# Kernel optimization log

Hardware: AMD Instinct MI355X
Metric: run time of the kernel (lower is better)

## Reference

```python
import jax, jax.numpy as jnp
import numpy as np

N, F_IN, H, C, E, G, OUT = 50000, 128, 4, 64, 800000, 128, 8

def _glorot(key, shape):
    lim = float(np.sqrt(6.0 / (shape[0] + shape[-1] if len(shape) == 2 else shape[-1] + 1)))
    return jax.random.uniform(key, shape, jnp.float32, -lim, lim)

def setup_inputs() -> dict:
    key = jax.random.key(0)
    ks = jax.random.split(key, 12)
    x = jax.random.normal(ks[0], (N, F_IN), jnp.float32)
    edge_index = jax.random.randint(ks[1], (2, E), 0, N, jnp.int64)
    batch = jnp.sort(jax.random.randint(ks[2], (N,), 0, G, jnp.int64))
    return {
        "x": x, "edge_index": edge_index, "batch": batch,
        "W1": _glorot(ks[3], (F_IN, H * C)),
        "a1s": _glorot(ks[4], (H, C)), "a1d": _glorot(ks[5], (H, C)),
        "b1": jnp.zeros((H * C,), jnp.float32),
        "W2": _glorot(ks[6], (H * C, H * C)),
        "a2s": _glorot(ks[7], (H, C)), "a2d": _glorot(ks[8], (H, C)),
        "b2": jnp.zeros((C,), jnp.float32),
        "fc_w": _glorot(ks[9], (C, OUT)),
        "fc_b": jnp.zeros((OUT,), jnp.float32),
    }

def _gat_conv(x, src, dst, W, a_src, a_dst, bias, concat):
    # x: [N, in]; src/dst: [E'] (self-loops already appended, PyG default)
    n = x.shape[0]
    h = (x @ W).reshape(n, H, C)                       # [N, H, C]
    alpha_src = (h * a_src).sum(-1)                    # [N, H]
    alpha_dst = (h * a_dst).sum(-1)                    # [N, H]
    e = alpha_src[src] + alpha_dst[dst]                # [E', H]
    e = jax.nn.leaky_relu(e, 0.2)
    # neighbor softmax grouped by destination node
    m = jax.ops.segment_max(e, dst, num_segments=n)    # [N, H]
    ex = jnp.exp(e - m[dst])
    denom = jax.ops.segment_sum(ex, dst, num_segments=n)
    alpha = ex / (denom[dst] + 1e-16)                  # [E', H]
    msg = h[src] * alpha[:, :, None]                   # [E', H, C]
    out = jax.ops.segment_sum(msg, dst, num_segments=n)  # [N, H, C]
    out = out.reshape(n, H * C) if concat else out.mean(axis=1)
    return out + bias

def reference(x, edge_index, batch, W1, a1s, a1d, b1, W2, a2s, a2d, b2, fc_w, fc_b):
    n = x.shape[0]
    loop = jnp.arange(n, dtype=edge_index.dtype)
    src = jnp.concatenate([edge_index[0], loop])
    dst = jnp.concatenate([edge_index[1], loop])
    h = _gat_conv(x, src, dst, W1, a1s, a1d, b1, concat=True)
    h = jax.nn.elu(h)                                  # activation, dropout p=0
    h = _gat_conv(h, src, dst, W2, a2s, a2d, b2, concat=False)
    # global mean pool over graphs
    sums = jax.ops.segment_sum(h, batch, num_segments=G)
    cnts = jax.ops.segment_sum(jnp.ones((n,), h.dtype), batch, num_segments=G)
    pooled = sums / jnp.maximum(cnts, 1.0)[:, None]    # [G, C]
    return pooled @ fc_w + fc_b                        # [G, OUT]
```

## Files before the change

kernel.cpp:

```cpp
#include <hip/hip_runtime.h>
#include <hip/hip_bf16.h>
#include <cstddef>
#include <cstdint>

#define NN 50000
#define MPAD 50048
#define F_IN 128
#define NH 4
#define NC 64
#define NE 800000
#define NG 128
#define NOUT 8
#define HC 256
#define EP (NE + NN)

typedef unsigned short ushort_t;
typedef _Float16 f16;
typedef __attribute__((ext_vector_type(2))) _Float16 f16x2;
typedef __attribute__((ext_vector_type(8))) _Float16 f16x8;
typedef __attribute__((ext_vector_type(4))) float f32x4;

__device__ __forceinline__ float lrelu02(float x) { return x > 0.0f ? x : 0.2f * x; }
__device__ __forceinline__ float elu1(float x)    { return x > 0.0f ? x : expm1f(x); }

__device__ __forceinline__ ushort_t f2h_bits(float f) {
    f16 h = (f16)f;
    union { f16 h; ushort_t u; } cv; cv.h = h;
    return cv.u;
}
__device__ __forceinline__ uint32_t pack2h(float a, float b) {
    union { f16 h[2]; uint32_t u; } cv;
    cv.h[0] = (f16)a; cv.h[1] = (f16)b;
    return cv.u;
}
__device__ __forceinline__ f16x2 as_h2(uint32_t q) {
    union { uint32_t u; f16x2 h; } cv; cv.u = q;
    return cv.h;
}
__device__ __forceinline__ void h2_unpack(uint32_t q, float& lo, float& hi) {
    union { uint32_t u; f16 h[2]; } cv; cv.u = q;
    lo = (float)cv.h[0];
    hi = (float)cv.h[1];
}

__device__ __forceinline__ float fdot2f(f16x2 a, f16x2 b, float c) {
#if __has_builtin(__builtin_amdgcn_fdot2)
    return __builtin_amdgcn_fdot2(a, b, c, false);
#else
    float d;
    asm("v_dot2_f32_f16 %0, %1, %2, %3" : "=v"(d) : "v"(a), "v"(b), "v"(c));
    return d;
#endif
}
__device__ __forceinline__ uint32_t permb(uint32_t a, uint32_t b, uint32_t s) {
    return __builtin_amdgcn_perm(a, b, s);
}
#define SEL_E 0x01000504u
#define SEL_O 0x03020706u

__device__ __forceinline__ void gld16(const void* g, void* l) {
    __builtin_amdgcn_global_load_lds(
        (const __attribute__((address_space(1))) unsigned int*)g,
        (__attribute__((address_space(3))) unsigned int*)l, 16, 0, 0);
}

#define XN4 (NN * F_IN / 4)
#define NW (F_IN * HC + HC * HC)
__global__ void prep_kernel(const int* __restrict__ edst,
                            const float* __restrict__ x,
                            const float* __restrict__ W1,
                            const float* __restrict__ W2,
                            int* __restrict__ deg,
                            f16* __restrict__ xh,
                            f16* __restrict__ w1t, f16* __restrict__ w2t) {
    int idx = blockIdx.x * blockDim.x + threadIdx.x;
    if (idx < EP) {
        int d = (idx < NE) ? edst[idx] : (idx - NE);
        atomicAdd(&deg[d], 1);
        return;
    }
    idx -= EP;
    if (idx < XN4) {
        float4 v = ((const float4*)x)[idx];
        f16 o[4] = {(f16)v.x, (f16)v.y, (f16)v.z, (f16)v.w};
        *(uint2*)(xh + idx * 4) = *(const uint2*)o;
        return;
    }
    idx -= XN4;
    const int n1 = F_IN * HC;
    if (idx < n1) {
        int k = idx / HC, n = idx % HC;
        w1t[n * F_IN + k] = (f16)W1[idx];
    } else if (idx < NW) {
        int i2 = idx - n1;
        int k = i2 / HC, n = i2 % HC;
        w2t[n * HC + k] = (f16)W2[i2];
    }
}

__global__ __launch_bounds__(256) void scan_p1(const int* __restrict__ deg,
                                               int* __restrict__ partials) {
    __shared__ int lds[256];
    int b = blockIdx.x, t = threadIdx.x;
    int i0 = b * 1024 + t * 4;
    int s = 0;
#pragma unroll
    for (int j = 0; j < 4; j++) { int i = i0 + j; if (i < NN) s += deg[i]; }
    lds[t] = s;
    __syncthreads();
    for (int o = 128; o; o >>= 1) { if (t < o) lds[t] += lds[t + o]; __syncthreads(); }
    if (t == 0) partials[b] = lds[0];
}

__global__ __launch_bounds__(256) void scan_p3(const int* __restrict__ deg,
                                               const int* __restrict__ partials,
                                               int* __restrict__ offs) {
    __shared__ int lds[256];
    __shared__ int base_s;
    int b = blockIdx.x, t = threadIdx.x;
    if (t == 0) {
        int s = 0;
        for (int i = 0; i < b; i++) s += partials[i];
        base_s = s;
        if (b == 0) offs[0] = 0;
    }
    int i0 = b * 1024 + t * 4;
    int v[4]; int s = 0;
#pragma unroll
    for (int j = 0; j < 4; j++) { int i = i0 + j; v[j] = (i < NN) ? deg[i] : 0; s += v[j]; }
    lds[t] = s;
    __syncthreads();
    for (int o = 1; o < 256; o <<= 1) {
        int x = (t >= o) ? lds[t - o] : 0;
        __syncthreads();
        lds[t] += x;
        __syncthreads();
    }
    int run = base_s + (lds[t] - s);
#pragma unroll
    for (int j = 0; j < 4; j++) { run += v[j]; int i = i0 + j; if (i < NN) offs[i + 1] = run; }
}

__global__ void edge_fill(const int* __restrict__ esrc, const int* __restrict__ edst,
                          const int* __restrict__ offs, int* __restrict__ fill,
                          int* __restrict__ csr) {
    int e = blockIdx.x * blockDim.x + threadIdx.x;
    if (e >= EP) return;
    int s, d;
    if (e < NE) { s = esrc[e]; d = edst[e]; } else { s = d = e - NE; }
    int pos = offs[d] + atomicAdd(&fill[d], 1);
    csr[pos] = s;
}

__global__ __launch_bounds__(256, 3) void gemm_gat(
        const f16* __restrict__ A, const f16* __restrict__ BT,
        const float* __restrict__ a_s, const float* __restrict__ a_d,
        ushort_t* __restrict__ hf2, float* __restrict__ asrc,
        float* __restrict__ adst, int M, int K) {
    __shared__ alignas(16) char smem[33792];
    f16* lA = (f16*)smem;
    f16* lB = (f16*)smem + 4096;

    int t = threadIdx.x;
    int wave = t >> 6, lane = t & 63;
    int wm = wave >> 1, wn = wave & 1;
    int quad = lane >> 4, l15 = lane & 15;
    int tileM = blockIdx.x * 128;
    int by = blockIdx.y;

    f32x4 acc[4][4];
#pragma unroll
    for (int f = 0; f < 4; f++)
#pragma unroll
        for (int g = 0; g < 4; g++) acc[f][g] = (f32x4){0.f, 0.f, 0.f, 0.f};

    for (int k0 = 0; k0 < K; k0 += 32) {
        __syncthreads();
#pragma unroll
        for (int i = 0; i < 2; i++) {
            int c = wave * 2 + i;
            int row = c * 16 + (lane >> 2);
            int kk = k0 + (lane & 3) * 8;
            gld16(A + (size_t)(tileM + row) * K + kk, &lA[c * 512]);
            gld16(BT + (size_t)(by * 128 + row) * K + kk, &lB[c * 512]);
        }
        __syncthreads();

        f16x8 ah[4], bh[4];
#pragma unroll
        for (int f = 0; f < 4; f++)
            ah[f] = *(const f16x8*)&lA[(wm * 64 + f * 16 + l15) * 32 + quad * 8];
#pragma unroll
        for (int g = 0; g < 4; g++)
            bh[g] = *(const f16x8*)&lB[(wn * 64 + g * 16 + l15) * 32 + quad * 8];
#pragma unroll
        for (int f = 0; f < 4; f++)
#pragma unroll
            for (int g = 0; g < 4; g++)
                acc[f][g] = __builtin_amdgcn_mfma_f32_16x16x32_f16(ah[f], bh[g], acc[f][g], 0, 0, 0);
    }

    int head = (by << 1) | wn;
    float as_v[4], ad_v[4];
#pragma unroll
    for (int g = 0; g < 4; g++) {
        as_v[g] = a_s[head * 64 + g * 16 + l15];
        ad_v[g] = a_d[head * 64 + g * 16 + l15];
    }
#pragma unroll
    for (int f = 0; f < 4; f++) {
#pragma unroll
        for (int r = 0; r < 4; r++) {
            float ps = acc[f][0][r] * as_v[0] + acc[f][1][r] * as_v[1]
                     + acc[f][2][r] * as_v[2] + acc[f][3][r] * as_v[3];
            float pd = acc[f][0][r] * ad_v[0] + acc[f][1][r] * ad_v[1]
                     + acc[f][2][r] * ad_v[2] + acc[f][3][r] * ad_v[3];
#pragma unroll
            for (int o = 1; o < 16; o <<= 1) {
                ps += __shfl_xor(ps, o);
                pd += __shfl_xor(pd, o);
            }
            int row = tileM + wm * 64 + f * 16 + quad * 4 + r;
            if (l15 == 0 && row < M) {
                asrc[row * 4 + head] = ps;
                adst[row * 4 + head] = pd;
            }
        }
    }

    __syncthreads();
    ushort_t* lC2u = (ushort_t*)smem;
    const uint32_t* lC2d = (const uint32_t*)smem;
#pragma unroll
    for (int f = 0; f < 4; f++)
#pragma unroll
        for (int g = 0; g < 4; g++)
#pragma unroll
            for (int r = 0; r < 4; r++)
                lC2u[(wm * 64 + f * 16 + quad * 4 + r) * 132 + (g * 16 + l15) * 2 + wn] =
                    f2h_bits(acc[f][g][r]);
    __syncthreads();
    uint32_t* hb2 = (uint32_t*)hf2;
#pragma unroll
    for (int it = 0; it < 32; it++) {
        int row = wave * 32 + it;
        uint32_t v = lC2d[row * 66 + lane];
        hb2[(size_t)(tileM + row) * 128 + by * 64 + lane] = v;
    }
}

template <int CONCAT>
__device__ void gat_node_fullwave(const ushort_t* __restrict__ hf2,
                                  const float* __restrict__ asrc,
                                  const float* __restrict__ adst,
                                  const int* __restrict__ offs,
                                  const int* __restrict__ csr,
                                  const float* __restrict__ bias,
                                  f16* __restrict__ oh,
                                  float* __restrict__ of,
                                  int node, int lane, uint2* lwF) {
    int start = offs[node];
    int deg = offs[node + 1] - start;
    float4 ad = *(const float4*)(adst + node * 4);

    float w0, w1, w2, w3;
    float m0, m1, m2, m3, i0, i1, i2, i3;
    int msrc = 0;

    if (deg <= 64) {
        float t0 = -1e30f, t1 = -1e30f, t2 = -1e30f, t3 = -1e30f;
        if (lane < deg) {
            int sidx = csr[start + lane];
            float4 as = *(const float4*)(asrc + sidx * 4);
            t0 = lrelu02(as.x + ad.x);
            t1 = lrelu02(as.y + ad.y);
            t2 = lrelu02(as.z + ad.z);
            t3 = lrelu02(as.w + ad.w);
            msrc = sidx;
        }
        m0 = t0; m1 = t1; m2 = t2; m3 = t3;
#pragma unroll
        for (int o = 1; o < 64; o <<= 1) {
            m0 = fmaxf(m0, __shfl_xor(m0, o));
            m1 = fmaxf(m1, __shfl_xor(m1, o));
            m2 = fmaxf(m2, __shfl_xor(m2, o));
            m3 = fmaxf(m3, __shfl_xor(m3, o));
        }
        w0 = __expf(t0 - m0);
        w1 = __expf(t1 - m1);
        w2 = __expf(t2 - m2);
        w3 = __expf(t3 - m3);
        float s0 = w0, s1 = w1, s2 = w2, s3 = w3;
#pragma unroll
        for (int o = 1; o < 64; o <<= 1) {
            s0 += __shfl_xor(s0, o);
            s1 += __shfl_xor(s1, o);
            s2 += __shfl_xor(s2, o);
            s3 += __shfl_xor(s3, o);
        }
        i0 = 1.0f / (s0 + 1e-16f);
        i1 = 1.0f / (s1 + 1e-16f);
        i2 = 1.0f / (s2 + 1e-16f);
        i3 = 1.0f / (s3 + 1e-16f);
        w0 *= i0; w1 *= i1; w2 *= i2; w3 *= i3;
    } else {
        m0 = m1 = m2 = m3 = -1e30f;
        float s0 = 0.f, s1 = 0.f, s2 = 0.f, s3 = 0.f;
        float e0 = 0.f, e1 = 0.f, e2 = 0.f, e3 = 0.f;
        for (int j = lane; j < deg; j += 64) {
            int sidx = csr[start + j];
            float4 as = *(const float4*)(asrc + sidx * 4);
            float t0 = lrelu02(as.x + ad.x);
            float t1 = lrelu02(as.y + ad.y);
            float t2 = lrelu02(as.z + ad.z);
            float t3 = lrelu02(as.w + ad.w);
            if (j == lane) { e0 = t0; e1 = t1; e2 = t2; e3 = t3; msrc = sidx; }
            float nm;
            nm = fmaxf(m0, t0); s0 = s0 * __expf(m0 - nm) + __expf(t0 - nm); m0 = nm;
            nm = fmaxf(m1, t1); s1 = s1 * __expf(m1 - nm) + __expf(t1 - nm); m1 = nm;
            nm = fmaxf(m2, t2); s2 = s2 * __expf(m2 - nm) + __expf(t2 - nm); m2 = nm;
            nm = fmaxf(m3, t3); s3 = s3 * __expf(m3 - nm) + __expf(t3 - nm); m3 = nm;
        }
        for (int o = 32; o; o >>= 1) {
            float om, os, nm;
            om = __shfl_xor(m0, o); os = __shfl_xor(s0, o);
            nm = fmaxf(m0, om); s0 = s0 * __expf(m0 - nm) + os * __expf(om - nm); m0 = nm;
            om = __shfl_xor(m1, o); os = __shfl_xor(s1, o);
            nm = fmaxf(m1, om); s1 = s1 * __expf(m1 - nm) + os * __expf(om - nm); m1 = nm;
            om = __shfl_xor(m2, o); os = __shfl_xor(s2, o);
            nm = fmaxf(m2, om); s2 = s2 * __expf(m2 - nm) + os * __expf(om - nm); m2 = nm;
            om = __shfl_xor(m3, o); os = __shfl_xor(s3, o);
            nm = fmaxf(m3, om); s3 = s3 * __expf(m3 - nm) + os * __expf(om - nm); m3 = nm;
        }
        i0 = 1.0f / (s0 + 1e-16f);
        i1 = 1.0f / (s1 + 1e-16f);
        i2 = 1.0f / (s2 + 1e-16f);
        i3 = 1.0f / (s3 + 1e-16f);
        w0 = __expf(e0 - m0) * i0;
        w1 = __expf(e1 - m1) * i1;
        w2 = __expf(e2 - m2) * i2;
        w3 = __expf(e3 - m3) * i3;
    }

    lwF[lane] = (uint2){pack2h(w0, w1), pack2h(w2, w3)};

    int hp = lane >> 5;
    const uint32_t* lwu = (const uint32_t*)lwF;
    float aE0 = 0.f, aO0 = 0.f, aE1 = 0.f, aO1 = 0.f;
    float c0a = 0.f, c0b = 0.f, c1a = 0.f, c1b = 0.f;
    const uint32_t* hb = (const uint32_t*)hf2 + lane * 2;
    int jmax = deg < 64 ? deg : 64;

    int j = 0;
    if (CONCAT) {
        for (; j + 4 <= jmax; j += 4) {
            int s0 = __builtin_amdgcn_readlane(msrc, j);
            int s1 = __builtin_amdgcn_readlane(msrc, j + 1);
            int s2 = __builtin_amdgcn_readlane(msrc, j + 2);
            int s3 = __builtin_amdgcn_readlane(msrc, j + 3);
            uint2 q0 = *(const uint2*)(hb + (size_t)s0 * 128);
            uint2 q1 = *(const uint2*)(hb + (size_t)s1 * 128);
            uint2 q2 = *(const uint2*)(hb + (size_t)s2 * 128);
            uint2 q3 = *(const uint2*)(hb + (size_t)s3 * 128);
            uint32_t wA = lwu[(j + 0) * 2 + hp];
            uint32_t wB = lwu[(j + 1) * 2 + hp];
            uint32_t wC = lwu[(j + 2) * 2 + hp];
            uint32_t wD = lwu[(j + 3) * 2 + hp];
            uint32_t weAB = permb(wA, wB, SEL_E), woAB = permb(wA, wB, SEL_O);
            uint32_t weCD = permb(wC, wD, SEL_E), woCD = permb(wC, wD, SEL_O);
            uint32_t xeAB = permb(q0.x, q1.x, SEL_E), xoAB = permb(q0.x, q1.x, SEL_O);
            uint32_t yeAB = permb(q0.y, q1.y, SEL_E), yoAB = permb(q0.y, q1.y, SEL_O);
            uint32_t xeCD = permb(q2.x, q3.x, SEL_E), xoCD = permb(q2.x, q3.x, SEL_O);
            uint32_t yeCD = permb(q2.y, q3.y, SEL_E), yoCD = permb(q2.y, q3.y, SEL_O);
            aE0 = fdot2f(as_h2(xeAB), as_h2(weAB), aE0);
            aO0 = fdot2f(as_h2(xoAB), as_h2(woAB), aO0);
            aE1 = fdot2f(as_h2(yeAB), as_h2(weAB), aE1);
            aO1 = fdot2f(as_h2(yoAB), as_h2(woAB), aO1);
            aE0 = fdot2f(as_h2(xeCD), as_h2(weCD), aE0);
            aO0 = fdot2f(as_h2(xoCD), as_h2(woCD), aO0);
            aE1 = fdot2f(as_h2(yeCD), as_h2(weCD), aE1);
            aO1 = fdot2f(as_h2(yoCD), as_h2(woCD), aO1);
        }
        for (; j < jmax; j++) {
            int sidx = __builtin_amdgcn_readlane(msrc, j);
            f16x2 wh = as_h2(lwu[j * 2 + hp]);
            uint2 q = *(const uint2*)(hb + (size_t)sidx * 128);
            f16x2 qx = as_h2(q.x), qy = as_h2(q.y);
            aE0 += (float)qx[0] * (float)wh[0];
            aO0 += (float)qx[1] * (float)wh[1];
            aE1 += (float)qy[0] * (float)wh[0];
            aO1 += (float)qy[1] * (float)wh[1];
        }
    } else {
        for (; j + 4 <= jmax; j += 4) {
            int s0 = __builtin_amdgcn_readlane(msrc, j);
            int s1 = __builtin_amdgcn_readlane(msrc, j + 1);
            int s2 = __builtin_amdgcn_readlane(msrc, j + 2);
            int s3 = __builtin_amdgcn_readlane(msrc, j + 3);
            uint2 q0 = *(const uint2*)(hb + (size_t)s0 * 128);
            uint2 q1 = *(const uint2*)(hb + (size_t)s1 * 128);
            uint2 q2 = *(const uint2*)(hb + (size_t)s2 * 128);
            uint2 q3 = *(const uint2*)(hb + (size_t)s3 * 128);
            f16x2 w0v = as_h2(lwu[(j + 0) * 2 + hp]);
            f16x2 w1v = as_h2(lwu[(j + 1) * 2 + hp]);
            f16x2 w2v = as_h2(lwu[(j + 2) * 2 + hp]);
            f16x2 w3v = as_h2(lwu[(j + 3) * 2 + hp]);
            c0a = fdot2f(as_h2(q0.x), w0v, c0a);
            c1a = fdot2f(as_h2(q0.y), w0v, c1a);
            c0b = fdot2f(as_h2(q1.x), w1v, c0b);
            c1b = fdot2f(as_h2(q1.y), w1v, c1b);
            c0a = fdot2f(as_h2(q2.x), w2v, c0a);
            c1a = fdot2f(as_h2(q2.y), w2v, c1a);
            c0b = fdot2f(as_h2(q3.x), w3v, c0b);
            c1b = fdot2f(as_h2(q3.y), w3v, c1b);
        }
        for (; j < jmax; j++) {
            int sidx = __builtin_amdgcn_readlane(msrc, j);
            f16x2 wh = as_h2(lwu[j * 2 + hp]);
            uint2 q = *(const uint2*)(hb + (size_t)sidx * 128);
            c0a = fdot2f(as_h2(q.x), wh, c0a);
            c1a = fdot2f(as_h2(q.y), wh, c1a);
        }
    }
    for (int jj = 64; jj < deg; jj++) {
        int sidx = csr[start + jj];
        float4 as = *(const float4*)(asrc + sidx * 4);
        float u0 = __expf(lrelu02(as.x + ad.x) - m0) * i0;
        float u1 = __expf(lrelu02(as.y + ad.y) - m1) * i1;
        float u2 = __expf(lrelu02(as.z + ad.z) - m2) * i2;
        float u3 = __expf(lrelu02(as.w + ad.w) - m3) * i3;
        float ue = hp ? u2 : u0;
        float uo = hp ? u3 : u1;
        uint2 q = *(const uint2*)(hb + (size_t)sidx * 128);
        float xl, xh2, yl, yh;
        h2_unpack(q.x, xl, xh2);
        h2_unpack(q.y, yl, yh);
        if (CONCAT) {
            aE0 += ue * xl;
            aO0 += uo * xh2;
            aE1 += ue * yl;
            aO1 += uo * yh;
        } else {
            c0a += ue * xl + uo * xh2;
            c1a += ue * yl + uo * yh;
        }
    }

    int c0 = (lane & 31) * 2;
    int he = hp * 2, ho = hp * 2 + 1;
    if (CONCAT) {
        size_t base = (size_t)node * HC;
        float vE0 = elu1(aE0 + bias[he * 64 + c0]);
        float vE1 = elu1(aE1 + bias[he * 64 + c0 + 1]);
        float vO0 = elu1(aO0 + bias[ho * 64 + c0]);
        float vO1 = elu1(aO1 + bias[ho * 64 + c0 + 1]);
        f16 pe[2] = {(f16)vE0, (f16)vE1};
        f16 po[2] = {(f16)vO0, (f16)vO1};
        *(uint32_t*)(oh + base + he * 64 + c0) = *(const uint32_t*)pe;
        *(uint32_t*)(oh + base + ho * 64 + c0) = *(const uint32_t*)po;
    } else {
        float s0 = c0a + c0b;
        float s1 = c1a + c1b;
        s0 += __shfl_xor(s0, 32);
        s1 += __shfl_xor(s1, 32);
        if (hp == 0) {
            float2 v = {0.25f * s0 + bias[c0], 0.25f * s1 + bias[c0 + 1]};
            *(float2*)(of + (size_t)node * NC + c0) = v;
        }
    }
}

template <int CONCAT>
__global__ __launch_bounds__(256) void gat_agg(const ushort_t* __restrict__ hf2,
                                               const float* __restrict__ asrc,
                                               const float* __restrict__ adst,
                                               const int* __restrict__ offs,
                                               const int* __restrict__ csr,
                                               const float* __restrict__ bias,
                                               f16* __restrict__ oh,
                                               float* __restrict__ of) {
    __shared__ uint4 lw4[4][64];
    int wave = threadIdx.x >> 6, lane = threadIdx.x & 63;
    int grp = lane >> 5, l31 = lane & 31;
    int hp = (lane >> 4) & 1;
    int nbase = blockIdx.x * 8 + wave * 2;
    int node = nbase + grp;
    int start = offs[node];
    int deg = offs[node + 1] - start;

    if (!__all(deg <= 32)) {
        uint2* lwF = (uint2*)&lw4[wave][0];
        gat_node_fullwave<CONCAT>(hf2, asrc, adst, offs, csr, bias, oh, of,
                                  nbase, lane, lwF);
        gat_node_fullwave<CONCAT>(hf2, asrc, adst, offs, csr, bias, oh, of,
                                  nbase + 1, lane, lwF);
        return;
    }

    float4 ad = *(const float4*)(adst + (size_t)node * 4);
    float t0 = -1e30f, t1 = -1e30f, t2 = -1e30f, t3 = -1e30f;
    int msrc = 0;
    if (l31 < deg) {
        int sidx = csr[start + l31];
        float4 as = *(const float4*)(asrc + (size_t)sidx * 4);
        t0 = lrelu02(as.x + ad.x);
        t1 = lrelu02(as.y + ad.y);
        t2 = lrelu02(as.z + ad.z);
        t3 = lrelu02(as.w + ad.w);
        msrc = sidx;
    }
    float m0 = t0, m1 = t1, m2 = t2, m3 = t3;
#pragma unroll
    for (int o = 1; o < 32; o <<= 1) {
        m0 = fmaxf(m0, __shfl_xor(m0, o));
        m1 = fmaxf(m1, __shfl_xor(m1, o));
        m2 = fmaxf(m2, __shfl_xor(m2, o));
        m3 = fmaxf(m3, __shfl_xor(m3, o));
    }
    float w0 = __expf(t0 - m0);
    float w1 = __expf(t1 - m1);
    float w2 = __expf(t2 - m2);
    float w3 = __expf(t3 - m3);
    float s0 = w0, s1 = w1, s2 = w2, s3 = w3;
#pragma unroll
    for (int o = 1; o < 32; o <<= 1) {
        s0 += __shfl_xor(s0, o);
        s1 += __shfl_xor(s1, o);
        s2 += __shfl_xor(s2, o);
        s3 += __shfl_xor(s3, o);
    }
    w0 *= 1.0f / (s0 + 1e-16f);
    w1 *= 1.0f / (s1 + 1e-16f);
    w2 *= 1.0f / (s2 + 1e-16f);
    w3 *= 1.0f / (s3 + 1e-16f);

    lw4[wave][lane] = (uint4){(uint32_t)msrc, pack2h(w0, w1),
                              (uint32_t)msrc, pack2h(w2, w3)};

    const uint2* lwp = (const uint2*)&lw4[wave][grp * 32];
    const uint4* hq = (const uint4*)hf2;
    int c0 = (l31 & 15) * 4;

    if (CONCAT) {
        float aE0 = 0.f, aE1 = 0.f, aE2 = 0.f, aE3 = 0.f;
        float aO0 = 0.f, aO1 = 0.f, aO2 = 0.f, aO3 = 0.f;
        int j = 0;
        for (; j + 2 <= deg; j += 2) {
            uint2 e0 = lwp[(j + 0) * 2 + hp];
            uint2 e1 = lwp[(j + 1) * 2 + hp];
            uint4 q0 = hq[(size_t)e0.x * 32 + l31];
            uint4 q1 = hq[(size_t)e1.x * 32 + l31];
            uint32_t we = permb(e0.y, e1.y, SEL_E);
            uint32_t wo = permb(e0.y, e1.y, SEL_O);
            aE0 = fdot2f(as_h2(permb(q0.x, q1.x, SEL_E)), as_h2(we), aE0);
            aO0 = fdot2f(as_h2(permb(q0.x, q1.x, SEL_O)), as_h2(wo), aO0);
            aE1 = fdot2f(as_h2(permb(q0.y, q1.y, SEL_E)), as_h2(we), aE1);
            aO1 = fdot2f(as_h2(permb(q0.y, q1.y, SEL_O)), as_h2(wo), aO1);
            aE2 = fdot2f(as_h2(permb(q0.z, q1.z, SEL_E)), as_h2(we), aE2);
            aO2 = fdot2f(as_h2(permb(q0.z, q1.z, SEL_O)), as_h2(wo), aO2);
            aE3 = fdot2f(as_h2(permb(q0.w, q1.w, SEL_E)), as_h2(we), aE3);
            aO3 = fdot2f(as_h2(permb(q0.w, q1.w, SEL_O)), as_h2(wo), aO3);
        }
        if (j < deg) {
            uint2 e0 = lwp[j * 2 + hp];
            uint4 q0 = hq[(size_t)e0.x * 32 + l31];
            f16x2 wh = as_h2(e0.y);
            f16x2 v;
            v = as_h2(q0.x); aE0 += (float)v[0] * (float)wh[0]; aO0 += (float)v[1] * (float)wh[1];
            v = as_h2(q0.y); aE1 += (float)v[0] * (float)wh[0]; aO1 += (float)v[1] * (float)wh[1];
            v = as_h2(q0.z); aE2 += (float)v[0] * (float)wh[0]; aO2 += (float)v[1] * (float)wh[1];
            v = as_h2(q0.w); aE3 += (float)v[0] * (float)wh[0]; aO3 += (float)v[1] * (float)wh[1];
        }
        int he = hp * 2, ho = hp * 2 + 1;
        size_t base = (size_t)node * HC;
        float4 bE = *(const float4*)(bias + he * 64 + c0);
        float4 bO = *(const float4*)(bias + ho * 64 + c0);
        f16 pe[4] = {(f16)elu1(aE0 + bE.x), (f16)elu1(aE1 + bE.y),
                     (f16)elu1(aE2 + bE.z), (f16)elu1(aE3 + bE.w)};
        f16 po[4] = {(f16)elu1(aO0 + bO.x), (f16)elu1(aO1 + bO.y),
                     (f16)elu1(aO2 + bO.z), (f16)elu1(aO3 + bO.w)};
        *(uint2*)(oh + base + he * 64 + c0) = *(const uint2*)pe;
        *(uint2*)(oh + base + ho * 64 + c0) = *(const uint2*)po;
    } else {
        float a0 = 0.f, a1 = 0.f, a2 = 0.f, a3 = 0.f;
        float b0 = 0.f, b1 = 0.f, b2 = 0.f, b3 = 0.f;
        int j = 0;
        for (; j + 2 <= deg; j += 2) {
            uint2 e0 = lwp[(j + 0) * 2 + hp];
            uint2 e1 = lwp[(j + 1) * 2 + hp];
            uint4 q0 = hq[(size_t)e0.x * 32 + l31];
            uint4 q1 = hq[(size_t)e1.x * 32 + l31];
            f16x2 wv0 = as_h2(e0.y), wv1 = as_h2(e1.y);
            a0 = fdot2f(as_h2(q0.x), wv0, a0);
            a1 = fdot2f(as_h2(q0.y), wv0, a1);
            a2 = fdot2f(as_h2(q0.z), wv0, a2);
            a3 = fdot2f(as_h2(q0.w), wv0, a3);
            b0 = fdot2f(as_h2(q1.x), wv1, b0);
            b1 = fdot2f(as_h2(q1.y), wv1, b1);
            b2 = fdot2f(as_h2(q1.z), wv1, b2);
            b3 = fdot2f(as_h2(q1.w), wv1, b3);
        }
        if (j < deg) {
            uint2 e0 = lwp[j * 2 + hp];
            uint4 q0 = hq[(size_t)e0.x * 32 + l31];
            f16x2 wv0 = as_h2(e0.y);
            a0 = fdot2f(as_h2(q0.x), wv0, a0);
            a1 = fdot2f(as_h2(q0.y), wv0, a1);
            a2 = fdot2f(as_h2(q0.z), wv0, a2);
            a3 = fdot2f(as_h2(q0.w), wv0, a3);
        }
        float u0 = a0 + b0, u1 = a1 + b1, u2 = a2 + b2, u3 = a3 + b3;
        u0 += __shfl_xor(u0, 16);
        u1 += __shfl_xor(u1, 16);
        u2 += __shfl_xor(u2, 16);
        u3 += __shfl_xor(u3, 16);
        if (hp == 0) {
            float4 bv = *(const float4*)(bias + c0);
            float4 v = {0.25f * u0 + bv.x, 0.25f * u1 + bv.y,
                        0.25f * u2 + bv.z, 0.25f * u3 + bv.w};
            *(float4*)(of + (size_t)node * NC + c0) = v;
        }
    }
}

__global__ __launch_bounds__(256) void pool_kernel(const float* __restrict__ out2,
                                                   const int* __restrict__ batch,
                                                   float* __restrict__ pool,
                                                   float* __restrict__ cnt) {
    int gw = (blockIdx.x * blockDim.x + threadIdx.x) >> 6;
    int lane = threadIdx.x & 63;
    int start = gw * 16;
    if (start >= NN) return;
    int end = start + 16 < NN ? start + 16 : NN;
    int curg = batch[start];
    float acc = 0.f; int run = 0;
    for (int node = start; node < end; node++) {
        int g = batch[node];
        if (g != curg) {
            atomicAdd(&pool[curg * 64 + lane], acc);
            if (lane == 0) atomicAdd(&cnt[curg], (float)run);
            curg = g; acc = 0.f; run = 0;
        }
        acc += out2[(size_t)node * NC + lane];
        run++;
    }
    atomicAdd(&pool[curg * 64 + lane], acc);
    if (lane == 0) atomicAdd(&cnt[curg], (float)run);
}

__global__ void fc_kernel(const float* __restrict__ pool, const float* __restrict__ cnt,
                          const float* __restrict__ fc_w, const float* __restrict__ fc_b,
                          float* __restrict__ out) {
    int idx = blockIdx.x * blockDim.x + threadIdx.x;
    if (idx >= NG * NOUT) return;
    int g = idx >> 3, o = idx & 7;
    float inv = 1.0f / fmaxf(cnt[g], 1.0f);
    float s = 0.f;
#pragma unroll
    for (int c = 0; c < 64; c++) s += pool[g * 64 + c] * fc_w[c * 8 + o];
    out[idx] = s * inv + fc_b[o];
}

extern "C" void kernel_launch(void* const* d_in, const int* in_sizes, int n_in,
                              void* d_out, int out_size, void* d_ws, size_t ws_size,
                              hipStream_t stream) {
    const float* x    = (const float*)d_in[0];
    const int*   ei   = (const int*)d_in[1];
    const int*   batch= (const int*)d_in[2];
    const float* W1   = (const float*)d_in[3];
    const float* a1s  = (const float*)d_in[4];
    const float* a1d  = (const float*)d_in[5];
    const float* b1   = (const float*)d_in[6];
    const float* W2   = (const float*)d_in[7];
    const float* a2s  = (const float*)d_in[8];
    const float* a2d  = (const float*)d_in[9];
    const float* b2   = (const float*)d_in[10];
    const float* fc_w = (const float*)d_in[11];
    const float* fc_b = (const float*)d_in[12];
    float* out = (float*)d_out;

    char* p = (char*)d_ws;
    auto alloc = [&](size_t bytes) -> char* {
        char* r = p; p += (bytes + 255) & ~(size_t)255; return r;
    };
    int*   deg     = (int*)alloc((size_t)NN * 4);
    int*   fill    = (int*)alloc((size_t)NN * 4);
    float* pool    = (float*)alloc((size_t)NG * 64 * 4);
    float* cnt     = (float*)alloc((size_t)NG * 4);
    size_t zero_bytes = (size_t)(p - (char*)d_ws);
    int*   offs    = (int*)alloc((size_t)(NN + 1) * 4);
    int*   partials= (int*)alloc(64 * 4);
    int*   csr     = (int*)alloc((size_t)EP * 4);
    float* asrc    = (float*)alloc((size_t)NN * 4 * 4);
    float* adst    = (float*)alloc((size_t)NN * 4 * 4);
    ushort_t* hf2  = (ushort_t*)alloc((size_t)MPAD * HC * 2);
    f16*   xh      = (f16*)alloc((size_t)MPAD * F_IN * 2);
    f16*   act     = (f16*)alloc((size_t)MPAD * HC * 2);
    f16*   w1t     = (f16*)alloc((size_t)HC * F_IN * 2);
    f16*   w2t     = (f16*)alloc((size_t)HC * HC * 2);
    float* out2    = (float*)xh;

    hipMemsetAsync(d_ws, 0, zero_bytes, stream);

    int prep_n = EP + XN4 + NW;
    prep_kernel<<<(prep_n + 255) / 256, 256, 0, stream>>>(
        ei + NE, x, W1, W2, deg, xh, w1t, w2t);
    scan_p1<<<49, 256, 0, stream>>>(deg, partials);
    scan_p3<<<49, 256, 0, stream>>>(deg, partials, offs);
    edge_fill<<<(EP + 255) / 256, 256, 0, stream>>>(ei, ei + NE, offs, fill, csr);

    dim3 gg((NN + 127) / 128, HC / 128);
    int nb8 = (NN + 7) / 8;

    gemm_gat<<<gg, 256, 0, stream>>>(xh, w1t, a1s, a1d, hf2, asrc, adst, NN, F_IN);
    gat_agg<1><<<nb8, 256, 0, stream>>>(hf2, asrc, adst, offs, csr, b1, act, nullptr);
    gemm_gat<<<gg, 256, 0, stream>>>(act, w2t, a2s, a2d, hf2, asrc, adst, NN, HC);
    gat_agg<0><<<nb8, 256, 0, stream>>>(hf2, asrc, adst, offs, csr, b2, nullptr, out2);
    pool_kernel<<<((NN + 15) / 16 + 3) / 4, 256, 0, stream>>>(out2, batch, pool, cnt);
    fc_kernel<<<(NG * NOUT + 255) / 256, 256, 0, stream>>>(pool, cnt, fc_w, fc_b, out);
}
```

Before: 370.6 us.

## Software-pipeline neighbor feature gathers in GAT aggregation with early prefetch

The first four neighbor feature rows are now gathered straight after the CSR index load, before the attention softmax runs, so their latency overlaps the softmax math. The aggregation loop is rewritten as a 4-deep pipeline that issues the next pair of gathers between FMA blocks. Padding slots get zero weight and index 0 so no tail loop is needed, at the cost of wasted loads on padded slots. An occupancy hint (launch_bounds 256,8) caps register use, which may cause spills given the extra live registers.

```diff
diff --git a/kernel.cpp b/kernel.cpp
--- a/kernel.cpp
+++ b/kernel.cpp
@@ -471,14 +471,14 @@
 }
 
 template <int CONCAT>
-__global__ __launch_bounds__(256) void gat_agg(const ushort_t* __restrict__ hf2,
-                                               const float* __restrict__ asrc,
-                                               const float* __restrict__ adst,
-                                               const int* __restrict__ offs,
-                                               const int* __restrict__ csr,
-                                               const float* __restrict__ bias,
-                                               f16* __restrict__ oh,
-                                               float* __restrict__ of) {
+__global__ __launch_bounds__(256, 8) void gat_agg(const ushort_t* __restrict__ hf2,
+                                                  const float* __restrict__ asrc,
+                                                  const float* __restrict__ adst,
+                                                  const int* __restrict__ offs,
+                                                  const int* __restrict__ csr,
+                                                  const float* __restrict__ bias,
+                                                  f16* __restrict__ oh,
+                                                  float* __restrict__ of) {
     __shared__ uint4 lw4[4][64];
     int wave = threadIdx.x >> 6, lane = threadIdx.x & 63;
     int grp = lane >> 5, l31 = lane & 31;
@@ -497,17 +497,29 @@
         return;
     }
 
+    const uint4* hq = (const uint4*)hf2;
+    int msrc = 0;
+    bool act = l31 < deg;
+    if (act) msrc = csr[start + l31];
+
+    int b0 = grp * 32;
+    int i0 = __shfl(msrc, b0 + 0);
+    int i1 = __shfl(msrc, b0 + 1);
+    int i2 = __shfl(msrc, b0 + 2);
+    int i3 = __shfl(msrc, b0 + 3);
+    uint4 q0 = hq[(uint32_t)i0 * 32u + l31];
+    uint4 q1 = hq[(uint32_t)i1 * 32u + l31];
+    uint4 q2 = hq[(uint32_t)i2 * 32u + l31];
+    uint4 q3 = hq[(uint32_t)i3 * 32u + l31];
+
     float4 ad = *(const float4*)(adst + (size_t)node * 4);
     float t0 = -1e30f, t1 = -1e30f, t2 = -1e30f, t3 = -1e30f;
-    int msrc = 0;
-    if (l31 < deg) {
-        int sidx = csr[start + l31];
-        float4 as = *(const float4*)(asrc + (size_t)sidx * 4);
+    if (act) {
+        float4 as = *(const float4*)(asrc + (size_t)msrc * 4);
         t0 = lrelu02(as.x + ad.x);
         t1 = lrelu02(as.y + ad.y);
         t2 = lrelu02(as.z + ad.z);
         t3 = lrelu02(as.w + ad.w);
-        msrc = sidx;
     }
     float m0 = t0, m1 = t1, m2 = t2, m3 = t3;
 #pragma unroll
@@ -538,38 +550,61 @@
                               (uint32_t)msrc, pack2h(w2, w3)};
 
     const uint2* lwp = (const uint2*)&lw4[wave][grp * 32];
-    const uint4* hq = (const uint4*)hf2;
     int c0 = (l31 & 15) * 4;
+    int deg4 = (deg + 3) & ~3;
+
+    uint32_t wy0 = lwp[0 * 2 + hp].y;
+    uint32_t wy1 = lwp[1 * 2 + hp].y;
+    uint32_t wy2 = lwp[2 * 2 + hp].y;
+    uint32_t wy3 = lwp[3 * 2 + hp].y;
 
     if (CONCAT) {
         float aE0 = 0.f, aE1 = 0.f, aE2 = 0.f, aE3 = 0.f;
         float aO0 = 0.f, aO1 = 0.f, aO2 = 0.f, aO3 = 0.f;
         int j = 0;
-        for (; j + 2 <= deg; j += 2) {
-            uint2 e0 = lwp[(j + 0) * 2 + hp];
-            uint2 e1 = lwp[(j + 1) * 2 + hp];
-            uint4 q0 = hq[(size_t)e0.x * 32 + l31];
-            uint4 q1 = hq[(size_t)e1.x * 32 + l31];
-            uint32_t we = permb(e0.y, e1.y, SEL_E);
-            uint32_t wo = permb(e0.y, e1.y, SEL_O);
-            aE0 = fdot2f(as_h2(permb(q0.x, q1.x, SEL_E)), as_h2(we), aE0);
-            aO0 = fdot2f(as_h2(permb(q0.x, q1.x, SEL_O)), as_h2(wo), aO0);
-            aE1 = fdot2f(as_h2(permb(q0.y, q1.y, SEL_E)), as_h2(we), aE1);
-            aO1 = fdot2f(as_h2(permb(q0.y, q1.y, SEL_O)), as_h2(wo), aO1);
-            aE2 = fdot2f(as_h2(permb(q0.z, q1.z, SEL_E)), as_h2(we), aE2);
-            aO2 = fdot2f(as_h2(permb(q0.z, q1.z, SEL_O)), as_h2(wo), aO2);
-            aE3 = fdot2f(as_h2(permb(q0.w, q1.w, SEL_E)), as_h2(we), aE3);
-            aO3 = fdot2f(as_h2(permb(q0.w, q1.w, SEL_O)), as_h2(wo), aO3);
-        }
-        if (j < deg) {
-            uint2 e0 = lwp[j * 2 + hp];
-            uint4 q0 = hq[(size_t)e0.x * 32 + l31];
-            f16x2 wh = as_h2(e0.y);
-            f16x2 v;
-            v = as_h2(q0.x); aE0 += (float)v[0] * (float)wh[0]; aO0 += (float)v[1] * (float)wh[1];
-            v = as_h2(q0.y); aE1 += (float)v[0] * (float)wh[0]; aO1 += (float)v[1] * (float)wh[1];
-            v = as_h2(q0.z); aE2 += (float)v[0] * (float)wh[0]; aO2 += (float)v[1] * (float)wh[1];
-            v = as_h2(q0.w); aE3 += (float)v[0] * (float)wh[0]; aO3 += (float)v[1] * (float)wh[1];
+        for (;;) {
+            int jn = j + 4;
+            bool more = jn < deg4;
+            {
+                uint32_t we = permb(wy0, wy1, SEL_E);
+                uint32_t wo = permb(wy0, wy1, SEL_O);
+                aE0 = fdot2f(as_h2(permb(q0.x, q1.x, SEL_E)), as_h2(we), aE0);
+                aO0 = fdot2f(as_h2(permb(q0.x, q1.x, SEL_O)), as_h2(wo), aO0);
+                aE1 = fdot2f(as_h2(permb(q0.y, q1.y, SEL_E)), as_h2(we), aE1);
+                aO1 = fdot2f(as_h2(permb(q0.y, q1.y, SEL_O)), as_h2(wo), aO1);
+                aE2 = fdot2f(as_h2(permb(q0.z, q1.z, SEL_E)), as_h2(we), aE2);
+                aO2 = fdot2f(as_h2(permb(q0.z, q1.z, SEL_O)), as_h2(wo), aO2);
+                aE3 = fdot2f(as_h2(permb(q0.w, q1.w, SEL_E)), as_h2(we), aE3);
+                aO3 = fdot2f(as_h2(permb(q0.w, q1.w, SEL_O)), as_h2(wo), aO3);
+            }
+            if (more) {
+                uint2 n0 = lwp[(jn + 0) * 2 + hp];
+                uint2 n1 = lwp[(jn + 1) * 2 + hp];
+                wy0 = n0.y; wy1 = n1.y;
+                q0 = hq[n0.x * 32u + l31];
+                q1 = hq[n1.x * 32u + l31];
+            }
+            {
+                uint32_t we = permb(wy2, wy3, SEL_E);
+                uint32_t wo = permb(wy2, wy3, SEL_O);
+                aE0 = fdot2f(as_h2(permb(q2.x, q3.x, SEL_E)), as_h2(we), aE0);
+                aO0 = fdot2f(as_h2(permb(q2.x, q3.x, SEL_O)), as_h2(wo), aO0);
+                aE1 = fdot2f(as_h2(permb(q2.y, q3.y, SEL_E)), as_h2(we), aE1);
+                aO1 = fdot2f(as_h2(permb(q2.y, q3.y, SEL_O)), as_h2(wo), aO1);
+                aE2 = fdot2f(as_h2(permb(q2.z, q3.z, SEL_E)), as_h2(we), aE2);
+                aO2 = fdot2f(as_h2(permb(q2.z, q3.z, SEL_O)), as_h2(wo), aO2);
+                aE3 = fdot2f(as_h2(permb(q2.w, q3.w, SEL_E)), as_h2(we), aE3);
+                aO3 = fdot2f(as_h2(permb(q2.w, q3.w, SEL_O)), as_h2(wo), aO3);
+            }
+            if (more) {
+                uint2 n2 = lwp[(jn + 2) * 2 + hp];
+                uint2 n3 = lwp[(jn + 3) * 2 + hp];
+                wy2 = n2.y; wy3 = n3.y;
+                q2 = hq[n2.x * 32u + l31];
+                q3 = hq[n3.x * 32u + l31];
+            }
+            if (!more) break;
+            j = jn;
         }
         int he = hp * 2, ho = hp * 2 + 1;
         size_t base = (size_t)node * HC;
@@ -583,33 +618,51 @@
         *(uint2*)(oh + base + ho * 64 + c0) = *(const uint2*)po;
     } else {
         float a0 = 0.f, a1 = 0.f, a2 = 0.f, a3 = 0.f;
-        float b0 = 0.f, b1 = 0.f, b2 = 0.f, b3 = 0.f;
+        float b0f = 0.f, b1f = 0.f, b2f = 0.f, b3f = 0.f;
         int j = 0;
-        for (; j + 2 <= deg; j += 2) {
-            uint2 e0 = lwp[(j + 0) * 2 + hp];
-            uint2 e1 = lwp[(j + 1) * 2 + hp];
-            uint4 q0 = hq[(size_t)e0.x * 32 + l31];
-            uint4 q1 = hq[(size_t)e1.x * 32 + l31];
-            f16x2 wv0 = as_h2(e0.y), wv1 = as_h2(e1.y);
-            a0 = fdot2f(as_h2(q0.x), wv0, a0);
-            a1 = fdot2f(as_h2(q0.y), wv0, a1);
-            a2 = fdot2f(as_h2(q0.z), wv0, a2);
-            a3 = fdot2f(as_h2(q0.w), wv0, a3);
-            b0 = fdot2f(as_h2(q1.x), wv1, b0);
-            b1 = fdot2f(as_h2(q1.y), wv1, b1);
-            b2 = fdot2f(as_h2(q1.z), wv1, b2);
-            b3 = fdot2f(as_h2(q1.w), wv1, b3);
-        }
-        if (j < deg) {
-            uint2 e0 = lwp[j * 2 + hp];
-            uint4 q0 = hq[(size_t)e0.x * 32 + l31];
-            f16x2 wv0 = as_h2(e0.y);
-            a0 = fdot2f(as_h2(q0.x), wv0, a0);
-            a1 = fdot2f(as_h2(q0.y), wv0, a1);
-            a2 = fdot2f(as_h2(q0.z), wv0, a2);
-            a3 = fdot2f(as_h2(q0.w), wv0, a3);
-        }
-        float u0 = a0 + b0, u1 = a1 + b1, u2 = a2 + b2, u3 = a3 + b3;
+        for (;;) {
+            int jn = j + 4;
+            bool more = jn < deg4;
+            {
+                f16x2 wvA = as_h2(wy0), wvB = as_h2(wy1);
+                a0 = fdot2f(as_h2(q0.x), wvA, a0);
+                a1 = fdot2f(as_h2(q0.y), wvA, a1);
+                a2 = fdot2f(as_h2(q0.z), wvA, a2);
+                a3 = fdot2f(as_h2(q0.w), wvA, a3);
+                b0f = fdot2f(as_h2(q1.x), wvB, b0f);
+                b1f = fdot2f(as_h2(q1.y), wvB, b1f);
+                b2f = fdot2f(as_h2(q1.z), wvB, b2f);
+                b3f = fdot2f(as_h2(q1.w), wvB, b3f);
+            }
+            if (more) {
+                uint2 n0 = lwp[(jn + 0) * 2 + hp];
+                uint2 n1 = lwp[(jn + 1) * 2 + hp];
+                wy0 = n0.y; wy1 = n1.y;
+                q0 = hq[n0.x * 32u + l31];
+                q1 = hq[n1.x * 32u + l31];
+            }
+            {
+                f16x2 wvC = as_h2(wy2), wvD = as_h2(wy3);
+                a0 = fdot2f(as_h2(q2.x), wvC, a0);
+                a1 = fdot2f(as_h2(q2.y), wvC, a1);
+                a2 = fdot2f(as_h2(q2.z), wvC, a2);
+                a3 = fdot2f(as_h2(q2.w), wvC, a3);
+                b0f = fdot2f(as_h2(q3.x), wvD, b0f);
+                b1f = fdot2f(as_h2(q3.y), wvD, b1f);
+                b2f = fdot2f(as_h2(q3.z), wvD, b2f);
+                b3f = fdot2f(as_h2(q3.w), wvD, b3f);
+            }
+            if (more) {
+                uint2 n2 = lwp[(jn + 2) * 2 + hp];
+                uint2 n3 = lwp[(jn + 3) * 2 + hp];
+                wy2 = n2.y; wy3 = n3.y;
+                q2 = hq[n2.x * 32u + l31];
+                q3 = hq[n3.x * 32u + l31];
+            }
+            if (!more) break;
+            j = jn;
+        }
+        float u0 = a0 + b0f, u1 = a1 + b1f, u2 = a2 + b2f, u3 = a3 + b3f;
         u0 += __shfl_xor(u0, 16);
         u1 += __shfl_xor(u1, 16);
         u2 += __shfl_xor(u2, 16);
```

Result: no change. 366.0 us (-1.3%).
